# Optimization experiments

Hardware: AMD Instinct MI355X
Metric: run time of the kernel (lower is better)

The kernel has to match this reference:

```python
import jax, jax.numpy as jnp
import numpy as np

EMBED_DIM = 1024
B, S = 4, 4096


def setup_inputs() -> dict:
    key = jax.random.key(0)
    kx, kq, kk, kv = jax.random.split(key, 4)
    x = jax.random.normal(kx, (B, S, EMBED_DIM), dtype=jnp.float32)
    W_Q = jax.random.normal(kq, (EMBED_DIM, EMBED_DIM), dtype=jnp.float32)
    W_K = jax.random.normal(kk, (EMBED_DIM, EMBED_DIM), dtype=jnp.float32)
    W_V = jax.random.normal(kv, (EMBED_DIM, EMBED_DIM), dtype=jnp.float32)
    return {"x": x, "W_Q": W_Q, "W_K": W_K, "W_V": W_V}


def reference(x, W_Q, W_K, W_V):
    # Q, K, V: [B, S, D]
    Q = x @ W_Q
    K = x @ W_K
    V = x @ W_V
    scale = 1.0 / jnp.sqrt(jnp.float32(EMBED_DIM))
    # scores: [B, S, S] (full score matrix, as in the original)
    scores = jnp.einsum('bsd,btd->bst', Q, K) * scale
    attn = jax.nn.softmax(scores, axis=-1)
    # output: [B, S, D]
    Z = jnp.einsum('bst,btd->bsd', attn, V)
    return Z
```

## Files before the change

kernel.cpp:

```cpp
#include <hip/hip_runtime.h>


typedef _Float16 half8 __attribute__((ext_vector_type(8)));
typedef _Float16 half4v __attribute__((ext_vector_type(4)));
typedef float floatx4 __attribute__((ext_vector_type(4)));

__device__ __forceinline__ void glds16(const _Float16* g, _Float16* l) {
    __builtin_amdgcn_global_load_lds(
        (const __attribute__((address_space(1))) void*)g,
        (__attribute__((address_space(3))) void*)l, 16, 0, 0);
}

__device__ __forceinline__ void stage_tile(_Float16* s, const _Float16* g,
                                           int ldg, int tid) {
    const int wb = (tid & 192) * 8;
    {
        const int c = tid;
        glds16(g + (size_t)(c >> 2) * ldg + (c & 3) * 8, s + wb);
    }
    {
        const int c = 256 + tid;
        glds16(g + (size_t)(c >> 2) * ldg + (c & 3) * 8, s + 2048 + wb);
    }
}

template <bool SPLITIN, int OMODE>
__global__ __launch_bounds__(256, 2) void gemm_nt(
    const _Float16* __restrict__ AH, const _Float16* __restrict__ AL,
    const _Float16* BH, const _Float16* BL,
    void* out0, void* out1,
    const float* __restrict__ rdiv, float scale, int M, int N, int K,
    const _Float16* BH2, const _Float16* BL2, void* o0b, void* o1b)
{
    if (blockIdx.z == 1) { BH = BH2; BL = BL2; out0 = o0b; out1 = o1b; }

    __shared__ _Float16 sAH[128 * 32];
    __shared__ _Float16 sBH[128 * 32];
    __shared__ _Float16 sAL[SPLITIN ? 128 * 32 : 8];
    __shared__ _Float16 sBL[SPLITIN ? 128 * 32 : 8];

    const int tid = threadIdx.x;
    const int bm = blockIdx.y, bn = blockIdx.x;
    const int lane = tid & 63, quad = lane >> 4, lrow = lane & 15;
    const int wave = tid >> 6, wm = wave >> 1, wn = wave & 1;

    const _Float16* Ab = AH + (size_t)bm * 128 * K;
    const _Float16* Bb = BH + (size_t)bn * 128 * K;
    const _Float16* AbL = SPLITIN ? (AL + (size_t)bm * 128 * K) : nullptr;
    const _Float16* BbL = SPLITIN ? (BL + (size_t)bn * 128 * K) : nullptr;

    floatx4 acc[4][4] = {};

    const int aoff = (wm * 64 + lrow) * 32 + quad * 8;
    const int boff = (wn * 64 + lrow) * 32 + quad * 8;

    for (int k0 = 0; k0 < K; k0 += 32) {
        stage_tile(sAH, Ab + k0, K, tid);
        stage_tile(sBH, Bb + k0, K, tid);
        if (SPLITIN) {
            stage_tile(sAL, AbL + k0, K, tid);
            stage_tile(sBL, BbL + k0, K, tid);
        }
        __syncthreads();

        half8 aH[4], bH[4], aL[4], bL[4];
        #pragma unroll
        for (int i = 0; i < 4; ++i) {
            aH[i] = *(const half8*)&sAH[aoff + i * 16 * 32];
            bH[i] = *(const half8*)&sBH[boff + i * 16 * 32];
            if (SPLITIN) {
                aL[i] = *(const half8*)&sAL[aoff + i * 16 * 32];
                bL[i] = *(const half8*)&sBL[boff + i * 16 * 32];
            }
        }
        #pragma unroll
        for (int mi = 0; mi < 4; ++mi)
            #pragma unroll
            for (int nj = 0; nj < 4; ++nj) {
                acc[mi][nj] = __builtin_amdgcn_mfma_f32_16x16x32_f16(
                    aH[mi], bH[nj], acc[mi][nj], 0, 0, 0);
                if (SPLITIN) {
                    acc[mi][nj] = __builtin_amdgcn_mfma_f32_16x16x32_f16(
                        aH[mi], bL[nj], acc[mi][nj], 0, 0, 0);
                    acc[mi][nj] = __builtin_amdgcn_mfma_f32_16x16x32_f16(
                        aL[mi], bH[nj], acc[mi][nj], 0, 0, 0);
                }
            }
        __syncthreads();
    }

    #pragma unroll
    for (int mi = 0; mi < 4; ++mi) {
        #pragma unroll
        for (int r = 0; r < 4; ++r) {
            const int grow = bm * 128 + wm * 64 + mi * 16 + quad * 4 + r;
            float s = scale;
            if (OMODE == 1) s = scale / rdiv[grow];
            #pragma unroll
            for (int nj = 0; nj < 4; ++nj) {
                const int gcol = bn * 128 + wn * 64 + nj * 16 + lrow;
                const float v = acc[mi][nj][r] * s;
                const size_t idx = (size_t)grow * N + gcol;
                if (OMODE <= 1) {
                    ((float*)out0)[idx] = v;
                } else if (OMODE == 2) {
                    ((_Float16*)out0)[idx] = (_Float16)v;
                } else {
                    const _Float16 h = (_Float16)v;
                    ((_Float16*)out0)[idx] = h;
                    ((_Float16*)out1)[idx] = (_Float16)(v - (float)h);
                }
            }
        }
    }
}

__global__ __launch_bounds__(256) void split_scale(
    const float* __restrict__ x, _Float16* __restrict__ hi,
    _Float16* __restrict__ lo, int n)
{
    int i = (blockIdx.x * 256 + threadIdx.x) * 4;
    const int stride = gridDim.x * 256 * 4;
    for (; i < n; i += stride) {
        float4 v = *(const float4*)(x + i);
        float a[4] = {v.x * 256.f, v.y * 256.f, v.z * 256.f, v.w * 256.f};
        half4v h, l;
        #pragma unroll
        for (int j = 0; j < 4; ++j) {
            h[j] = (_Float16)a[j];
            l[j] = (_Float16)(a[j] - (float)h[j]);
        }
        *(half4v*)(hi + i) = h;
        *(half4v*)(lo + i) = l;
    }
}

__global__ __launch_bounds__(256) void wprep(
    const float* __restrict__ W, _Float16* __restrict__ hiT,
    _Float16* __restrict__ loT, int dim)
{
    __shared__ float t[32][33];
    const int n0 = blockIdx.x * 32, k0 = blockIdx.y * 32;
    const int tx = threadIdx.x, ty = threadIdx.y;
    #pragma unroll
    for (int i = 0; i < 4; ++i)
        t[ty + 8 * i][tx] = 256.f * W[(size_t)(k0 + ty + 8 * i) * dim + n0 + tx];
    __syncthreads();
    #pragma unroll
    for (int i = 0; i < 4; ++i) {
        const int nn = ty + 8 * i;
        const float v = t[tx][nn];
        const _Float16 h = (_Float16)v;
        const size_t o = (size_t)(n0 + nn) * dim + k0 + tx;
        hiT[o] = h;
        if (loT) loT[o] = (_Float16)(v - (float)h);
    }
}

__global__ __launch_bounds__(256) void softmax_p(
    const float* __restrict__ Sc, _Float16* __restrict__ P,
    float* __restrict__ rowsum)
{
    __shared__ float red[8];
    const int tid = threadIdx.x;
    const float* row = Sc + (size_t)blockIdx.x * 4096;
    _Float16* prow = P + (size_t)blockIdx.x * 4096;

    float m = -1e30f;
    for (int c = tid * 4; c < 4096; c += 1024) {
        float4 v = *(const float4*)(row + c);
        m = fmaxf(m, fmaxf(fmaxf(v.x, v.y), fmaxf(v.z, v.w)));
    }
    #pragma unroll
    for (int off = 32; off; off >>= 1) m = fmaxf(m, __shfl_xor(m, off, 64));
    if ((tid & 63) == 0) red[tid >> 6] = m;
    __syncthreads();
    const float rmax = fmaxf(fmaxf(red[0], red[1]), fmaxf(red[2], red[3]));

    float s = 0.f;
    for (int c = tid * 4; c < 4096; c += 1024) {
        float4 v = *(const float4*)(row + c);
        float p0 = __expf(v.x - rmax), p1 = __expf(v.y - rmax);
        float p2 = __expf(v.z - rmax), p3 = __expf(v.w - rmax);
        s += p0 + p1 + p2 + p3;
        half4v h = {(_Float16)p0, (_Float16)p1, (_Float16)p2, (_Float16)p3};
        *(half4v*)(prow + c) = h;
    }
    #pragma unroll
    for (int off = 32; off; off >>= 1) s += __shfl_xor(s, off, 64);
    __syncthreads();
    if ((tid & 63) == 0) red[4 + (tid >> 6)] = s;
    __syncthreads();
    if (tid == 0) rowsum[blockIdx.x] = red[4] + red[5] + red[6] + red[7];
}

extern "C" void kernel_launch(void* const* d_in, const int* in_sizes, int n_in,
                              void* d_out, int out_size, void* d_ws, size_t ws_size,
                              hipStream_t stream) {
    const int Bb = 4, S = 4096, D = 1024;
    const size_t SD = (size_t)S * D;
    const size_t SS = (size_t)S * S;

    const float* x  = (const float*)d_in[0];
    const float* WQ = (const float*)d_in[1];
    const float* WK = (const float*)d_in[2];
    const float* WV = (const float*)d_in[3];
    float* out = (float*)d_out;

    char* w = (char*)d_ws;
    _Float16* WQhT = (_Float16*)w;  w += (size_t)D * D * 2;
    _Float16* WQlT = (_Float16*)w;  w += (size_t)D * D * 2;
    _Float16* WKhT = (_Float16*)w;  w += (size_t)D * D * 2;
    _Float16* WKlT = (_Float16*)w;  w += (size_t)D * D * 2;
    _Float16* WvhT = (_Float16*)w;  w += (size_t)D * D * 2;
    _Float16* xhi  = (_Float16*)w;  w += SD * 2;
    _Float16* xlo  = (_Float16*)w;  w += SD * 2;
    _Float16* Qhi  = (_Float16*)w;  w += SD * 2;
    _Float16* Qlo  = (_Float16*)w;  w += SD * 2;
    _Float16* Khi  = (_Float16*)w;  w += SD * 2;
    _Float16* Klo  = (_Float16*)w;  w += SD * 2;
    _Float16* VT   = (_Float16*)w;  w += SD * 2;
    float*    rowsum = (float*)w;   w += (size_t)S * 4;
    float*    Sc   = (float*)w;     w += SS * 4;
    _Float16* P    = (_Float16*)w;  w += SS * 2;

    const float kInv256 = 0.00390625f;
    const float kScScale = 4.76837158203125e-7f;

    dim3 blk(256);

    wprep<<<dim3(32, 32), dim3(32, 8), 0, stream>>>(WQ, WQhT, WQlT, D);
    wprep<<<dim3(32, 32), dim3(32, 8), 0, stream>>>(WK, WKhT, WKlT, D);
    wprep<<<dim3(32, 32), dim3(32, 8), 0, stream>>>(WV, WvhT, nullptr, D);

    for (int b = 0; b < Bb; ++b) {
        const float* xb = x + (size_t)b * SD;
        float* outb = out + (size_t)b * SD;

        split_scale<<<dim3(4096), blk, 0, stream>>>(xb, xhi, xlo, (int)SD);

        gemm_nt<true, 3><<<dim3(D / 128, S / 128, 2), blk, 0, stream>>>(
            xhi, xlo, WQhT, WQlT, Qhi, Qlo, nullptr, kInv256, S, D, D,
            WKhT, WKlT, Khi, Klo);

        gemm_nt<false, 2><<<dim3(S / 128, D / 128, 1), blk, 0, stream>>>(
            WvhT, nullptr, xhi, nullptr, VT, nullptr, nullptr, kInv256,
            D, S, D, nullptr, nullptr, nullptr, nullptr);

        gemm_nt<true, 0><<<dim3(S / 128, S / 128, 1), blk, 0, stream>>>(
            Qhi, Qlo, Khi, Klo, Sc, nullptr, nullptr, kScScale, S, S, D,
            nullptr, nullptr, nullptr, nullptr);

        softmax_p<<<dim3(S), blk, 0, stream>>>(Sc, P, rowsum);

        gemm_nt<false, 1><<<dim3(D / 128, S / 128, 1), blk, 0, stream>>>(
            P, nullptr, VT, nullptr, outb, nullptr, rowsum, kInv256, S, D, S,
            nullptr, nullptr, nullptr, nullptr);
    }
}
```

Before: 1.333 ms.

## Fuse row-max partials into score GEMM epilogue, merge weight prep launches

The QK^T GEMM epilogue now computes per-row partial maxima over each wave's 64-column slice and writes them to a small buffer. The softmax kernel reduces those 64 partials instead of making a separate full pass over the 64 MB score row data to find the max. The three weight-prep launches are merged into one via blockIdx.z, and the GEMM loads use precomputed incremented pointers instead of recomputing addresses each k-step. This saves one full read of the score matrix per batch at the cost of extra shuffles and stores in the GEMM epilogue.

Result: no change. 1.312 ms (-1.6%).

```diff
diff --git a/kernel.cpp b/kernel.cpp
--- a/kernel.cpp
+++ b/kernel.cpp
@@ -11,25 +11,13 @@
         (__attribute__((address_space(3))) void*)l, 16, 0, 0);
 }
 
-__device__ __forceinline__ void stage_tile(_Float16* s, const _Float16* g,
-                                           int ldg, int tid) {
-    const int wb = (tid & 192) * 8;
-    {
-        const int c = tid;
-        glds16(g + (size_t)(c >> 2) * ldg + (c & 3) * 8, s + wb);
-    }
-    {
-        const int c = 256 + tid;
-        glds16(g + (size_t)(c >> 2) * ldg + (c & 3) * 8, s + 2048 + wb);
-    }
-}
-
-template <bool SPLITIN, int OMODE>
+template <bool SPLITIN, int OMODE, bool PMAX>
 __global__ __launch_bounds__(256, 2) void gemm_nt(
     const _Float16* __restrict__ AH, const _Float16* __restrict__ AL,
     const _Float16* BH, const _Float16* BL,
     void* out0, void* out1,
-    const float* __restrict__ rdiv, float scale, int M, int N, int K,
+    const float* __restrict__ rdiv, float* __restrict__ pmax,
+    float scale, int M, int N, int K,
     const _Float16* BH2, const _Float16* BL2, void* o0b, void* o1b)
 {
     if (blockIdx.z == 1) { BH = BH2; BL = BL2; out0 = o0b; out1 = o1b; }
@@ -44,10 +32,17 @@
     const int lane = tid & 63, quad = lane >> 4, lrow = lane & 15;
     const int wave = tid >> 6, wm = wave >> 1, wn = wave & 1;
 
-    const _Float16* Ab = AH + (size_t)bm * 128 * K;
-    const _Float16* Bb = BH + (size_t)bn * 128 * K;
-    const _Float16* AbL = SPLITIN ? (AL + (size_t)bm * 128 * K) : nullptr;
-    const _Float16* BbL = SPLITIN ? (BL + (size_t)bn * 128 * K) : nullptr;
+    const int wb = (tid & 192) * 8;
+    const size_t g0 = (size_t)(tid >> 2) * K + (tid & 3) * 8;
+    const size_t g1 = (size_t)((256 + tid) >> 2) * K + (tid & 3) * 8;
+    const _Float16* pA0 = AH + (size_t)bm * 128 * K + g0;
+    const _Float16* pA1 = AH + (size_t)bm * 128 * K + g1;
+    const _Float16* pB0 = BH + (size_t)bn * 128 * K + g0;
+    const _Float16* pB1 = BH + (size_t)bn * 128 * K + g1;
+    const _Float16* pA0L = SPLITIN ? (AL + (size_t)bm * 128 * K + g0) : nullptr;
+    const _Float16* pA1L = SPLITIN ? (AL + (size_t)bm * 128 * K + g1) : nullptr;
+    const _Float16* pB0L = SPLITIN ? (BL + (size_t)bn * 128 * K + g0) : nullptr;
+    const _Float16* pB1L = SPLITIN ? (BL + (size_t)bn * 128 * K + g1) : nullptr;
 
     floatx4 acc[4][4] = {};
 
@@ -55,12 +50,14 @@
     const int boff = (wn * 64 + lrow) * 32 + quad * 8;
 
     for (int k0 = 0; k0 < K; k0 += 32) {
-        stage_tile(sAH, Ab + k0, K, tid);
-        stage_tile(sBH, Bb + k0, K, tid);
+        glds16(pA0, sAH + wb);        glds16(pA1, sAH + 2048 + wb);
+        glds16(pB0, sBH + wb);        glds16(pB1, sBH + 2048 + wb);
         if (SPLITIN) {
-            stage_tile(sAL, AbL + k0, K, tid);
-            stage_tile(sBL, BbL + k0, K, tid);
-        }
+            glds16(pA0L, sAL + wb);   glds16(pA1L, sAL + 2048 + wb);
+            glds16(pB0L, sBL + wb);   glds16(pB1L, sBL + 2048 + wb);
+        }
+        pA0 += 32; pA1 += 32; pB0 += 32; pB1 += 32;
+        if (SPLITIN) { pA0L += 32; pA1L += 32; pB0L += 32; pB1L += 32; }
         __syncthreads();
 
         half8 aH[4], bH[4], aL[4], bL[4];
@@ -96,19 +93,28 @@
             const int grow = bm * 128 + wm * 64 + mi * 16 + quad * 4 + r;
             float s = scale;
             if (OMODE == 1) s = scale / rdiv[grow];
+            float v[4];
+            #pragma unroll
+            for (int nj = 0; nj < 4; ++nj) v[nj] = acc[mi][nj][r] * s;
+            if (PMAX) {
+                float mx = fmaxf(fmaxf(v[0], v[1]), fmaxf(v[2], v[3]));
+                #pragma unroll
+                for (int off = 1; off < 16; off <<= 1)
+                    mx = fmaxf(mx, __shfl_xor(mx, off));
+                if (lrow == 0) pmax[(size_t)grow * 64 + bn * 2 + wn] = mx;
+            }
             #pragma unroll
             for (int nj = 0; nj < 4; ++nj) {
                 const int gcol = bn * 128 + wn * 64 + nj * 16 + lrow;
-                const float v = acc[mi][nj][r] * s;
                 const size_t idx = (size_t)grow * N + gcol;
                 if (OMODE <= 1) {
-                    ((float*)out0)[idx] = v;
+                    ((float*)out0)[idx] = v[nj];
                 } else if (OMODE == 2) {
-                    ((_Float16*)out0)[idx] = (_Float16)v;
+                    ((_Float16*)out0)[idx] = (_Float16)v[nj];
                 } else {
-                    const _Float16 h = (_Float16)v;
+                    const _Float16 h = (_Float16)v[nj];
                     ((_Float16*)out0)[idx] = h;
-                    ((_Float16*)out1)[idx] = (_Float16)(v - (float)h);
+                    ((_Float16*)out1)[idx] = (_Float16)(v[nj] - (float)h);
                 }
             }
         }
@@ -135,10 +141,18 @@
     }
 }
 
-__global__ __launch_bounds__(256) void wprep(
-    const float* __restrict__ W, _Float16* __restrict__ hiT,
-    _Float16* __restrict__ loT, int dim)
-{
+__global__ __launch_bounds__(256) void wprep3(
+    const float* __restrict__ W0, const float* __restrict__ W1,
+    const float* __restrict__ W2,
+    _Float16* __restrict__ h0, _Float16* __restrict__ l0,
+    _Float16* __restrict__ h1, _Float16* __restrict__ l1,
+    _Float16* __restrict__ h2, int dim)
+{
+    const int z = blockIdx.z;
+    const float* W = (z == 0) ? W0 : (z == 1) ? W1 : W2;
+    _Float16* hiT = (z == 0) ? h0 : (z == 1) ? h1 : h2;
+    _Float16* loT = (z == 0) ? l0 : (z == 1) ? l1 : nullptr;
+
     __shared__ float t[32][33];
     const int n0 = blockIdx.x * 32, k0 = blockIdx.y * 32;
     const int tx = threadIdx.x, ty = threadIdx.y;
@@ -158,28 +172,27 @@
 }
 
 __global__ __launch_bounds__(256) void softmax_p(
-    const float* __restrict__ Sc, _Float16* __restrict__ P,
-    float* __restrict__ rowsum)
+    const float* __restrict__ Sc, const float* __restrict__ pmax,
+    _Float16* __restrict__ P, float* __restrict__ rowsum)
 {
     __shared__ float red[8];
     const int tid = threadIdx.x;
-    const float* row = Sc + (size_t)blockIdx.x * 4096;
-    _Float16* prow = P + (size_t)blockIdx.x * 4096;
-
-    float m = -1e30f;
-    for (int c = tid * 4; c < 4096; c += 1024) {
-        float4 v = *(const float4*)(row + c);
-        m = fmaxf(m, fmaxf(fmaxf(v.x, v.y), fmaxf(v.z, v.w)));
-    }
-    #pragma unroll
-    for (int off = 32; off; off >>= 1) m = fmaxf(m, __shfl_xor(m, off, 64));
-    if ((tid & 63) == 0) red[tid >> 6] = m;
+    const int row = blockIdx.x;
+    const float* srow = Sc + (size_t)row * 4096;
+    _Float16* prow = P + (size_t)row * 4096;
+
+    if (tid < 64) {
+        float m = pmax[(size_t)row * 64 + tid];
+        #pragma unroll
+        for (int off = 32; off; off >>= 1) m = fmaxf(m, __shfl_xor(m, off));
+        if (tid == 0) red[0] = m;
+    }
     __syncthreads();
-    const float rmax = fmaxf(fmaxf(red[0], red[1]), fmaxf(red[2], red[3]));
+    const float rmax = red[0];
 
     float s = 0.f;
     for (int c = tid * 4; c < 4096; c += 1024) {
-        float4 v = *(const float4*)(row + c);
+        float4 v = *(const float4*)(srow + c);
         float p0 = __expf(v.x - rmax), p1 = __expf(v.y - rmax);
         float p2 = __expf(v.z - rmax), p3 = __expf(v.w - rmax);
         s += p0 + p1 + p2 + p3;
@@ -188,10 +201,9 @@
     }
     #pragma unroll
     for (int off = 32; off; off >>= 1) s += __shfl_xor(s, off, 64);
-    __syncthreads();
     if ((tid & 63) == 0) red[4 + (tid >> 6)] = s;
     __syncthreads();
-    if (tid == 0) rowsum[blockIdx.x] = red[4] + red[5] + red[6] + red[7];
+    if (tid == 0) rowsum[row] = red[4] + red[5] + red[6] + red[7];
 }
 
 extern "C" void kernel_launch(void* const* d_in, const int* in_sizes, int n_in,
@@ -221,6 +233,7 @@
     _Float16* Klo  = (_Float16*)w;  w += SD * 2;
     _Float16* VT   = (_Float16*)w;  w += SD * 2;
     float*    rowsum = (float*)w;   w += (size_t)S * 4;
+    float*    pmax = (float*)w;     w += (size_t)S * 64 * 4;
     float*    Sc   = (float*)w;     w += SS * 4;
     _Float16* P    = (_Float16*)w;  w += SS * 2;
 
@@ -229,9 +242,8 @@
 
     dim3 blk(256);
 
-    wprep<<<dim3(32, 32), dim3(32, 8), 0, stream>>>(WQ, WQhT, WQlT, D);
-    wprep<<<dim3(32, 32), dim3(32, 8), 0, stream>>>(WK, WKhT, WKlT, D);
-    wprep<<<dim3(32, 32), dim3(32, 8), 0, stream>>>(WV, WvhT, nullptr, D);
+    wprep3<<<dim3(32, 32, 3), dim3(32, 8), 0, stream>>>(
+        WQ, WK, WV, WQhT, WQlT, WKhT, WKlT, WvhT, D);
 
     for (int b = 0; b < Bb; ++b) {
         const float* xb = x + (size_t)b * SD;
@@ -239,22 +251,22 @@
 
         split_scale<<<dim3(4096), blk, 0, stream>>>(xb, xhi, xlo, (int)SD);
 
-        gemm_nt<true, 3><<<dim3(D / 128, S / 128, 2), blk, 0, stream>>>(
-            xhi, xlo, WQhT, WQlT, Qhi, Qlo, nullptr, kInv256, S, D, D,
+        gemm_nt<true, 3, false><<<dim3(D / 128, S / 128, 2), blk, 0, stream>>>(
+            xhi, xlo, WQhT, WQlT, Qhi, Qlo, nullptr, nullptr, kInv256, S, D, D,
             WKhT, WKlT, Khi, Klo);
 
-        gemm_nt<false, 2><<<dim3(S / 128, D / 128, 1), blk, 0, stream>>>(
-            WvhT, nullptr, xhi, nullptr, VT, nullptr, nullptr, kInv256,
+        gemm_nt<false, 2, false><<<dim3(S / 128, D / 128, 1), blk, 0, stream>>>(
+            WvhT, nullptr, xhi, nullptr, VT, nullptr, nullptr, nullptr, kInv256,
             D, S, D, nullptr, nullptr, nullptr, nullptr);
 
-        gemm_nt<true, 0><<<dim3(S / 128, S / 128, 1), blk, 0, stream>>>(
-            Qhi, Qlo, Khi, Klo, Sc, nullptr, nullptr, kScScale, S, S, D,
+        gemm_nt<true, 0, true><<<dim3(S / 128, S / 128, 1), blk, 0, stream>>>(
+            Qhi, Qlo, Khi, Klo, Sc, nullptr, nullptr, pmax, kScScale, S, S, D,
             nullptr, nullptr, nullptr, nullptr);
 
-        softmax_p<<<dim3(S), blk, 0, stream>>>(Sc, P, rowsum);
-
-        gemm_nt<false, 1><<<dim3(D / 128, S / 128, 1), blk, 0, stream>>>(
-            P, nullptr, VT, nullptr, outb, nullptr, rowsum, kInv256, S, D, S,
-            nullptr, nullptr, nullptr, nullptr);
-    }
-}
+        softmax_p<<<dim3(S), blk, 0, stream>>>(Sc, pmax, P, rowsum);
+
+        gemm_nt<false, 1, false><<<dim3(D / 128, S / 128, 1), blk, 0, stream>>>(
+            P, nullptr, VT, nullptr, outb, nullptr, rowsum, nullptr, kInv256,
+            S, D, S, nullptr, nullptr, nullptr, nullptr);
+    }
+}
```
